# Performance work log

Hardware: AMD Instinct MI355X
Metric: run time of the kernel (lower is better)

## Reference

```python
import jax, jax.numpy as jnp
import numpy as np

B, D, NB = 262144, 64, 1000


def setup_inputs() -> dict:
    key = jax.random.key(0)
    k1, k2, k3, k4 = jax.random.split(key, 4)
    x = jax.random.normal(k1, (B, D), dtype=jnp.float32)
    # per-dim sorted grid (mimics fit_marginals' linspace over extended data range)
    lo = -3.0 + 0.5 * jax.random.normal(k2, (D, 1))
    hi = 3.0 + 0.5 * jax.random.normal(k3, (D, 1))
    t = jnp.linspace(0.0, 1.0, NB, dtype=jnp.float32)[None, :]
    x_values = (lo + (hi - lo) * t).astype(jnp.float32)  # [D, NB], sorted per row
    # strictly increasing empirical CDF in (1e-6, 1-1e-6)
    w = jax.nn.softmax(jax.random.normal(k4, (D, NB)), axis=1)
    cdf = jnp.cumsum(w, axis=1)
    cdf = jnp.clip(cdf / cdf[:, -1:], 1e-6, 1.0 - 1e-6).astype(jnp.float32)
    return {"x": x, "x_values": x_values, "cdf_values": cdf}


def reference(x, x_values, cdf_values):
    """MarginalGaussianization.forward: per-dim CDF lookup + Phi^{-1}, with log-det."""
    nb = x_values.shape[1]
    xT = x.T  # [D, B]
    # vectorized per-dim binary search (replaces the Python loop over dims)
    idx = jax.vmap(lambda xv, xd: jnp.searchsorted(xv, xd, side='left'))(x_values, xT)
    idx = jnp.clip(idx, 1, nb - 1)  # [D, B]
    g = lambda tab, i: jnp.take_along_axis(tab, i, axis=1)
    x_l, x_r = g(x_values, idx - 1), g(x_values, idx)
    c_l, c_r = g(cdf_values, idx - 1), g(cdf_values, idx)
    denom = x_r - x_l + 1e-12
    u = c_l + (c_r - c_l) * (xT - x_l) / denom          # _cdf_and_pdf: no weight clamp
    p_hat = jnp.maximum((c_r - c_l) / denom, 1e-12)
    u = jnp.clip(u, 1e-6, 1.0 - 1e-6)
    # inverse Gaussian CDF
    e = jnp.clip(2.0 * u - 1.0, -0.99999, 0.99999)
    z = jnp.clip(jnp.sqrt(2.0) * jax.scipy.special.erfinv(e), -10.0, 10.0)  # [D, B]
    inv_sqrt_2pi = 1.0 / jnp.sqrt(2.0 * jnp.pi)
    phi = inv_sqrt_2pi * jnp.exp(-0.5 * z * z)
    log_det = jnp.sum(jnp.log(p_hat) - jnp.log(phi + 1e-12), axis=0)  # [B]
    return z.T, log_det
```

## Files before the change

kernel.cpp:

```cpp
#include <hip/hip_runtime.h>
#include <math.h>

#define NBINS 1000
#define NDIM 64
#define DIMS_PER_BLOCK 8
#define DIM_GROUPS (NDIM / DIMS_PER_BLOCK)
#define BLOCK_THREADS 1024
#define ROWS_PER_ITER (BLOCK_THREADS / 2)
#define ROW_BLOCKS 64

__global__ __launch_bounds__(1024) void mg_zero(float* __restrict__ p, int n) {
    int i = blockIdx.x * blockDim.x + threadIdx.x;
    if (i < n) p[i] = 0.0f;
}

__global__ __launch_bounds__(256) void mg_reduce(const float* __restrict__ ws,
                                                 float* __restrict__ out, int B) {
    int row = blockIdx.x * blockDim.x + threadIdx.x;
    if (row >= B) return;
    float s = 0.0f;
#pragma unroll
    for (int g = 0; g < DIM_GROUPS; ++g) s += ws[(size_t)g * B + row];
    out[row] = s;
}

#define DIM_MATH(xd_, base_, i_, a_, b_, sc_, php_, ss_, zout_)                   \
    {                                                                             \
        float xd = (xd_);                                                         \
        int i = (i_);                                                             \
        float2 a = (a_), b = (b_);                                                \
        if (__builtin_expect((xd > b.x && i < NBINS - 2) ||                       \
                             (xd <= a.x && i > 0), 0)) {                          \
            while (xd > b.x && i < NBINS - 2) {                                   \
                ++i; a = b; b = knots[(base_) + i + 1];                           \
            }                                                                     \
            while (xd <= a.x && i > 0) {                                          \
                --i; b = a; a = knots[(base_) + i];                               \
            }                                                                     \
        }                                                                         \
        float slope = (b.y - a.y) * (sc_);                                        \
        float u = fmaf(slope, xd - a.x, a.y);                                     \
        float ph = fmaxf(slope, 1e-12f);                                          \
        float e1 = fminf(fmaxf(fmaf(2.0f, u, -1.0f), -0.99999f), 0.99999f);       \
        float wv = -0.6931471805599453f *                                         \
                   __builtin_amdgcn_logf(fmaf(-e1, e1, 1.0f));                    \
        float t = wv - 2.5f;                                                      \
        float p = 2.81022636e-08f;                                                \
        p = fmaf(p, t, 3.43273939e-07f);                                          \
        p = fmaf(p, t, -3.5233877e-06f);                                          \
        p = fmaf(p, t, -4.39150654e-06f);                                         \
        p = fmaf(p, t, 0.00021858087f);                                           \
        p = fmaf(p, t, -0.00125372503f);                                          \
        p = fmaf(p, t, -0.00417768164f);                                          \
        p = fmaf(p, t, 0.246640727f);                                             \
        p = fmaf(p, t, 1.50140941f);                                              \
        if (wv >= 5.0f) {                                                         \
            float tq = sqrtf(wv) - 3.0f;                                          \
            float pt = -0.000200214257f;                                          \
            pt = fmaf(pt, tq, 0.000100950558f);                                   \
            pt = fmaf(pt, tq, 0.00134934322f);                                    \
            pt = fmaf(pt, tq, -0.00367342844f);                                   \
            pt = fmaf(pt, tq, 0.00573950773f);                                    \
            pt = fmaf(pt, tq, -0.0076224613f);                                    \
            pt = fmaf(pt, tq, 0.00943887047f);                                    \
            pt = fmaf(pt, tq, 1.00167406f);                                       \
            pt = fmaf(pt, tq, 2.83297682f);                                       \
            p = pt;                                                               \
        }                                                                         \
        float z = 1.4142135623730951f * p * e1;   \
        (zout_) = z;                                                              \
        (ss_) = fmaf(z, z, (ss_));                                                \
        (php_) *= ph;                                                             \
    }

__device__ __forceinline__ float pair_swap_dpp(float v) {
    return __int_as_float(__builtin_amdgcn_update_dpp(
        __float_as_int(v), __float_as_int(v), 0xB1, 0xF, 0xF, true));
}

template <bool USE_WS>
__global__ __launch_bounds__(BLOCK_THREADS, 8)
void mg_main(const float* __restrict__ x,
             const float* __restrict__ xvals,
             const float* __restrict__ cdf,
             float* __restrict__ out, float* __restrict__ ws, int B) {
    __shared__ float2 knots[DIMS_PER_BLOCK * NBINS];

    const int dimbase = blockIdx.y * DIMS_PER_BLOCK;

    {
        const float4* xv4 = (const float4*)(xvals + (size_t)dimbase * NBINS);
        const float4* cd4 = (const float4*)(cdf + (size_t)dimbase * NBINS);
        for (int k = threadIdx.x; k < DIMS_PER_BLOCK * NBINS / 4; k += BLOCK_THREADS) {
            float4 a = xv4[k], c = cd4[k];
            knots[k * 4 + 0] = make_float2(a.x, c.x);
            knots[k * 4 + 1] = make_float2(a.y, c.y);
            knots[k * 4 + 2] = make_float2(a.z, c.z);
            knots[k * 4 + 3] = make_float2(a.w, c.w);
        }
    }
    __syncthreads();

    const int dl = (threadIdx.x & 1) * 4;
    const int qidx = blockIdx.y * 2 + (threadIdx.x & 1);

    float scale[4], bias[4];
#pragma unroll
    for (int j = 0; j < 4; ++j) {
        float l = knots[(dl + j) * NBINS].x;
        float h = knots[(dl + j) * NBINS + NBINS - 1].x;
        float s = (float)(NBINS - 1) / (h - l);
        scale[j] = s;
        bias[j] = -l * s;
    }

    const int rstride = gridDim.x * ROWS_PER_ITER;
    int row = blockIdx.x * ROWS_PER_ITER + (threadIdx.x >> 1);

    float4 xq = make_float4(0.f, 0.f, 0.f, 0.f);
    float4 xn = make_float4(0.f, 0.f, 0.f, 0.f);
    if (row < B) xq = ((const float4*)x)[(size_t)row * (NDIM / 4) + qidx];
    if (row + rstride < B)
        xn = ((const float4*)x)[(size_t)(row + rstride) * (NDIM / 4) + qidx];

    int ii[4];
    float2 kl[4], kr[4];
    {
        float xv[4] = {xq.x, xq.y, xq.z, xq.w};
#pragma unroll
        for (int j = 0; j < 4; ++j) {
            int i = (int)fmaf(xv[j], scale[j], bias[j]);
            ii[j] = min(max(i, 0), NBINS - 2);
        }
#pragma unroll
        for (int j = 0; j < 4; ++j) {
            kl[j] = knots[(dl + j) * NBINS + ii[j]];
            kr[j] = knots[(dl + j) * NBINS + ii[j] + 1];
        }
    }

    for (; row < B; row += rstride) {
        const int prow = row + 2 * rstride;
        float4 xn2 = make_float4(0.f, 0.f, 0.f, 0.f);
        if (prow < B) xn2 = ((const float4*)x)[(size_t)prow * (NDIM / 4) + qidx];

        float z4[4], php = 1.0f, sumsq = 0.0f;
        DIM_MATH(xq.x, (dl + 0) * NBINS, ii[0], kl[0], kr[0], scale[0],
                 php, sumsq, z4[0]);
        DIM_MATH(xq.y, (dl + 1) * NBINS, ii[1], kl[1], kr[1], scale[1],
                 php, sumsq, z4[1]);
        DIM_MATH(xq.z, (dl + 2) * NBINS, ii[2], kl[2], kr[2], scale[2],
                 php, sumsq, z4[2]);
        DIM_MATH(xq.w, (dl + 3) * NBINS, ii[3], kl[3], kr[3], scale[3],
                 php, sumsq, z4[3]);

        {
            float xv[4] = {xn.x, xn.y, xn.z, xn.w};
#pragma unroll
            for (int j = 0; j < 4; ++j) {
                int i = (int)fmaf(xv[j], scale[j], bias[j]);
                ii[j] = min(max(i, 0), NBINS - 2);
            }
#pragma unroll
            for (int j = 0; j < 4; ++j) {
                kl[j] = knots[(dl + j) * NBINS + ii[j]];
                kr[j] = knots[(dl + j) * NBINS + ii[j] + 1];
            }
        }

        ((float4*)out)[(size_t)row * (NDIM / 4) + qidx] =
            make_float4(z4[0], z4[1], z4[2], z4[3]);

        float term = fmaf(0.5f, sumsq, 4.0f * 0.9189385332046727f) +
                     0.6931471805599453f * __builtin_amdgcn_logf(php);

        term += pair_swap_dpp(term);
        if ((threadIdx.x & 1) == 0) {
            if constexpr (USE_WS)
                ws[(size_t)blockIdx.y * B + row] = term;
            else
                atomicAdd(out + (size_t)B * NDIM + row, term);
        }

        xq = xn;
        xn = xn2;
    }
}

extern "C" void kernel_launch(void* const* d_in, const int* in_sizes, int n_in,
                              void* d_out, int out_size, void* d_ws, size_t ws_size,
                              hipStream_t stream) {
    const float* x = (const float*)d_in[0];
    const float* xvals = (const float*)d_in[1];
    const float* cdf = (const float*)d_in[2];
    float* out = (float*)d_out;
    int B = in_sizes[0] / NDIM;

    const size_t ws_need = (size_t)DIM_GROUPS * B * sizeof(float);
    dim3 grid(ROW_BLOCKS, DIM_GROUPS);

    if (ws_size >= ws_need) {
        float* ws = (float*)d_ws;
        hipLaunchKernelGGL((mg_main<true>), grid, dim3(BLOCK_THREADS), 0, stream,
                           x, xvals, cdf, out, ws, B);
        hipLaunchKernelGGL(mg_reduce, dim3((B + 255) / 256), dim3(256), 0, stream,
                           ws, out + (size_t)B * NDIM, B);
    } else {
        hipLaunchKernelGGL(mg_zero, dim3((B + 1023) / 1024), dim3(1024), 0, stream,
                           out + (size_t)B * NDIM, B);
        hipLaunchKernelGGL((mg_main<false>), grid, dim3(BLOCK_THREADS), 0, stream,
                           x, xvals, cdf, out, (float*)nullptr, B);
    }
}
```

Measured before the change: 138.0 us.

## Process two rows per thread per iteration and prescale CDF table to 2c-1

Each thread now handles two rows (A and B, half a block apart) per loop iteration, giving more independent work for instruction-level parallelism in place of the earlier software-pipelined knot prefetch. The CDF values are stored in shared memory as 2c-1, which removes one FMA per dimension. The log-det constant and the slope clamp are adjusted to account for the factor of two. Prefetch is now one iteration ahead instead of two, and register pressure rises, which may hurt occupancy.

```diff
diff --git a/kernel.cpp b/kernel.cpp
--- a/kernel.cpp
+++ b/kernel.cpp
@@ -6,7 +6,8 @@
 #define DIMS_PER_BLOCK 8
 #define DIM_GROUPS (NDIM / DIMS_PER_BLOCK)
 #define BLOCK_THREADS 1024
-#define ROWS_PER_ITER (BLOCK_THREADS / 2)
+#define ROWS_PER_ITER 1024
+#define ROW_HALF 512
 #define ROW_BLOCKS 64
 
 __global__ __launch_bounds__(1024) void mg_zero(float* __restrict__ p, int n) {
@@ -38,10 +39,10 @@
                 --i; b = a; a = knots[(base_) + i];                               \
             }                                                                     \
         }                                                                         \
-        float slope = (b.y - a.y) * (sc_);                                        \
-        float u = fmaf(slope, xd - a.x, a.y);                                     \
-        float ph = fmaxf(slope, 1e-12f);                                          \
-        float e1 = fminf(fmaxf(fmaf(2.0f, u, -1.0f), -0.99999f), 0.99999f);       \
+        float slope2 = (b.y - a.y) * (sc_);     \
+        float e = fmaf(slope2, xd - a.x, a.y);                                    \
+        float ph2 = fmaxf(slope2, 2e-12f);                                        \
+        float e1 = fminf(fmaxf(e, -0.99999f), 0.99999f);                          \
         float wv = -0.6931471805599453f *                                         \
                    __builtin_amdgcn_logf(fmaf(-e1, e1, 1.0f));                    \
         float t = wv - 2.5f;                                                      \
@@ -70,7 +71,7 @@
         float z = 1.4142135623730951f * p * e1;   \
         (zout_) = z;                                                              \
         (ss_) = fmaf(z, z, (ss_));                                                \
-        (php_) *= ph;                                                             \
+        (php_) *= ph2;                                                            \
     }
 
 __device__ __forceinline__ float pair_swap_dpp(float v) {
@@ -93,10 +94,10 @@
         const float4* cd4 = (const float4*)(cdf + (size_t)dimbase * NBINS);
         for (int k = threadIdx.x; k < DIMS_PER_BLOCK * NBINS / 4; k += BLOCK_THREADS) {
             float4 a = xv4[k], c = cd4[k];
-            knots[k * 4 + 0] = make_float2(a.x, c.x);
-            knots[k * 4 + 1] = make_float2(a.y, c.y);
-            knots[k * 4 + 2] = make_float2(a.z, c.z);
-            knots[k * 4 + 3] = make_float2(a.w, c.w);
+            knots[k * 4 + 0] = make_float2(a.x, fmaf(2.0f, c.x, -1.0f));
+            knots[k * 4 + 1] = make_float2(a.y, fmaf(2.0f, c.y, -1.0f));
+            knots[k * 4 + 2] = make_float2(a.z, fmaf(2.0f, c.z, -1.0f));
+            knots[k * 4 + 3] = make_float2(a.w, fmaf(2.0f, c.w, -1.0f));
         }
     }
     __syncthreads();
@@ -115,75 +116,86 @@
     }
 
     const int rstride = gridDim.x * ROWS_PER_ITER;
-    int row = blockIdx.x * ROWS_PER_ITER + (threadIdx.x >> 1);
-
-    float4 xq = make_float4(0.f, 0.f, 0.f, 0.f);
-    float4 xn = make_float4(0.f, 0.f, 0.f, 0.f);
-    if (row < B) xq = ((const float4*)x)[(size_t)row * (NDIM / 4) + qidx];
-    if (row + rstride < B)
-        xn = ((const float4*)x)[(size_t)(row + rstride) * (NDIM / 4) + qidx];
-
-    int ii[4];
-    float2 kl[4], kr[4];
-    {
-        float xv[4] = {xq.x, xq.y, xq.z, xq.w};
+    int rA = blockIdx.x * ROWS_PER_ITER + (threadIdx.x >> 1);
+
+    float4 xqA = make_float4(0.f, 0.f, 0.f, 0.f);
+    float4 xqB = make_float4(0.f, 0.f, 0.f, 0.f);
+    if (rA < B) xqA = ((const float4*)x)[(size_t)rA * (NDIM / 4) + qidx];
+    if (rA + ROW_HALF < B)
+        xqB = ((const float4*)x)[(size_t)(rA + ROW_HALF) * (NDIM / 4) + qidx];
+
+    for (; rA < B; rA += rstride) {
+        const int rB = rA + ROW_HALF;
+        const int pA = rA + rstride, pB = rB + rstride;
+        float4 xnA = make_float4(0.f, 0.f, 0.f, 0.f);
+        float4 xnB = make_float4(0.f, 0.f, 0.f, 0.f);
+        if (pA < B) xnA = ((const float4*)x)[(size_t)pA * (NDIM / 4) + qidx];
+        if (pB < B) xnB = ((const float4*)x)[(size_t)pB * (NDIM / 4) + qidx];
+
+        int iA[4], iB[4];
+        float2 klA[4], krA[4], klB[4], krB[4];
 #pragma unroll
         for (int j = 0; j < 4; ++j) {
-            int i = (int)fmaf(xv[j], scale[j], bias[j]);
-            ii[j] = min(max(i, 0), NBINS - 2);
+            int i = (int)fmaf(((const float*)&xqA)[j], scale[j], bias[j]);
+            iA[j] = min(max(i, 0), NBINS - 2);
+            i = (int)fmaf(((const float*)&xqB)[j], scale[j], bias[j]);
+            iB[j] = min(max(i, 0), NBINS - 2);
         }
 #pragma unroll
         for (int j = 0; j < 4; ++j) {
-            kl[j] = knots[(dl + j) * NBINS + ii[j]];
-            kr[j] = knots[(dl + j) * NBINS + ii[j] + 1];
-        }
-    }
-
-    for (; row < B; row += rstride) {
-        const int prow = row + 2 * rstride;
-        float4 xn2 = make_float4(0.f, 0.f, 0.f, 0.f);
-        if (prow < B) xn2 = ((const float4*)x)[(size_t)prow * (NDIM / 4) + qidx];
-
-        float z4[4], php = 1.0f, sumsq = 0.0f;
-        DIM_MATH(xq.x, (dl + 0) * NBINS, ii[0], kl[0], kr[0], scale[0],
-                 php, sumsq, z4[0]);
-        DIM_MATH(xq.y, (dl + 1) * NBINS, ii[1], kl[1], kr[1], scale[1],
-                 php, sumsq, z4[1]);
-        DIM_MATH(xq.z, (dl + 2) * NBINS, ii[2], kl[2], kr[2], scale[2],
-                 php, sumsq, z4[2]);
-        DIM_MATH(xq.w, (dl + 3) * NBINS, ii[3], kl[3], kr[3], scale[3],
-                 php, sumsq, z4[3]);
-
-        {
-            float xv[4] = {xn.x, xn.y, xn.z, xn.w};
-#pragma unroll
-            for (int j = 0; j < 4; ++j) {
-                int i = (int)fmaf(xv[j], scale[j], bias[j]);
-                ii[j] = min(max(i, 0), NBINS - 2);
+            klA[j] = knots[(dl + j) * NBINS + iA[j]];
+            krA[j] = knots[(dl + j) * NBINS + iA[j] + 1];
+        }
+#pragma unroll
+        for (int j = 0; j < 4; ++j) {
+            klB[j] = knots[(dl + j) * NBINS + iB[j]];
+            krB[j] = knots[(dl + j) * NBINS + iB[j] + 1];
+        }
+
+        float zA[4], zB[4];
+        float phpA = 1.0f, ssA = 0.0f, phpB = 1.0f, ssB = 0.0f;
+        DIM_MATH(xqA.x, (dl + 0) * NBINS, iA[0], klA[0], krA[0], scale[0],
+                 phpA, ssA, zA[0]);
+        DIM_MATH(xqA.y, (dl + 1) * NBINS, iA[1], klA[1], krA[1], scale[1],
+                 phpA, ssA, zA[1]);
+        DIM_MATH(xqA.z, (dl + 2) * NBINS, iA[2], klA[2], krA[2], scale[2],
+                 phpA, ssA, zA[2]);
+        DIM_MATH(xqA.w, (dl + 3) * NBINS, iA[3], klA[3], krA[3], scale[3],
+                 phpA, ssA, zA[3]);
+        DIM_MATH(xqB.x, (dl + 0) * NBINS, iB[0], klB[0], krB[0], scale[0],
+                 phpB, ssB, zB[0]);
+        DIM_MATH(xqB.y, (dl + 1) * NBINS, iB[1], klB[1], krB[1], scale[1],
+                 phpB, ssB, zB[1]);
+        DIM_MATH(xqB.z, (dl + 2) * NBINS, iB[2], klB[2], krB[2], scale[2],
+                 phpB, ssB, zB[2]);
+        DIM_MATH(xqB.w, (dl + 3) * NBINS, iB[3], klB[3], krB[3], scale[3],
+                 phpB, ssB, zB[3]);
+
+        ((float4*)out)[(size_t)rA * (NDIM / 4) + qidx] =
+            make_float4(zA[0], zA[1], zA[2], zA[3]);
+        if (rB < B)
+            ((float4*)out)[(size_t)rB * (NDIM / 4) + qidx] =
+                make_float4(zB[0], zB[1], zB[2], zB[3]);
+
+        float termA = fmaf(0.5f, ssA, 4.0f * 0.22579135264472744f) +
+                      0.6931471805599453f * __builtin_amdgcn_logf(phpA);
+        float termB = fmaf(0.5f, ssB, 4.0f * 0.22579135264472744f) +
+                      0.6931471805599453f * __builtin_amdgcn_logf(phpB);
+
+        termA += pair_swap_dpp(termA);
+        termB += pair_swap_dpp(termB);
+        if ((threadIdx.x & 1) == 0) {
+            if constexpr (USE_WS) {
+                ws[(size_t)blockIdx.y * B + rA] = termA;
+                if (rB < B) ws[(size_t)blockIdx.y * B + rB] = termB;
+            } else {
+                atomicAdd(out + (size_t)B * NDIM + rA, termA);
+                if (rB < B) atomicAdd(out + (size_t)B * NDIM + rB, termB);
             }
-#pragma unroll
-            for (int j = 0; j < 4; ++j) {
-                kl[j] = knots[(dl + j) * NBINS + ii[j]];
-                kr[j] = knots[(dl + j) * NBINS + ii[j] + 1];
-            }
-        }
-
-        ((float4*)out)[(size_t)row * (NDIM / 4) + qidx] =
-            make_float4(z4[0], z4[1], z4[2], z4[3]);
-
-        float term = fmaf(0.5f, sumsq, 4.0f * 0.9189385332046727f) +
-                     0.6931471805599453f * __builtin_amdgcn_logf(php);
-
-        term += pair_swap_dpp(term);
-        if ((threadIdx.x & 1) == 0) {
-            if constexpr (USE_WS)
-                ws[(size_t)blockIdx.y * B + row] = term;
-            else
-                atomicAdd(out + (size_t)B * NDIM + row, term);
-        }
-
-        xq = xn;
-        xn = xn2;
+        }
+
+        xqA = xnA;
+        xqB = xnB;
     }
 }
 
```

Measured after the change: 203.7 us. +47.6%, slower.
